# Kernel optimization log

Hardware: AMD Instinct MI355X
Metric: run time of the kernel (lower is better)

## Reference

```python
import jax, jax.numpy as jnp
import numpy as np

TOKENS, HIDDEN, N_EXPERTS = 16384, 2048, 64
JITTER_EPS = 0.01
Z_LOSS_COEFF = 0.001


def setup_inputs() -> dict:
    key = jax.random.key(0)
    k1, k2 = jax.random.split(key)
    x = jax.random.normal(k1, (TOKENS, HIDDEN), dtype=jnp.float32)
    w = jax.random.normal(k2, (N_EXPERTS, HIDDEN), dtype=jnp.float32) * 0.02  # router weight [E,H]
    return {"x": x, "w": w}


def _route_pass(scores_sel, scores, jitter_eps):
    # scores_sel: logits possibly with -inf at already-selected expert (top-2 pass)
    # scores:     original logits (used for abs/clamp factor, as in torch code)
    mx = jnp.max(scores_sel, axis=-1, keepdims=True)                      # [N,1]
    factor = jnp.maximum(jnp.abs(scores), mx)                             # scores.abs().clamp(min=mx)
    mask = jax.lax.stop_gradient((mx - scores) / factor > 2.0 * jitter_eps)
    masked_logits = jnp.where(mask, -jnp.inf, scores_sel)
    # eval path (training=False): selected_experts = argmax of (masked-for-selection) scores
    sel = jnp.argmax(scores_sel, axis=-1)[..., None]                      # [N,1] int
    gates = jax.nn.softmax(masked_logits, axis=-1)
    # mask_for_one: selected == argmax(gates) holds deterministically in eval -> 1.0
    mult = jnp.take_along_axis(gates, sel, axis=-1)                       # [N,1]
    return mult, sel


def reference(x, w):
    logits = x @ w.T                                                      # [N,E]
    # z-loss (identity on logits in forward; scalar returned for completeness)
    z_loss = Z_LOSS_COEFF * jnp.mean(jnp.square(jax.nn.logsumexp(logits, axis=-1)))
    original_gates = jax.nn.softmax(logits, axis=-1)
    # top-1 pass
    m1, s1 = _route_pass(logits, logits, JITTER_EPS)
    # top-2 pass: mask out the first selection
    e_idx = jnp.arange(logits.shape[-1])[None, :]
    scores2 = jnp.where(e_idx == s1, -jnp.inf, logits)
    m2, s2 = _route_pass(scores2, logits, JITTER_EPS)
    multiplier = jnp.concatenate([m1, m2], axis=-1)                       # [N,2]
    selected_experts = jnp.concatenate([s1, s2], axis=-1)                 # [N,2]
    return multiplier, original_gates, selected_experts, z_loss
```

## Files before the change

kernel.cpp:

```cpp
#include <hip/hip_runtime.h>
#include <math.h>

#define TOKENS 16384
#define HIDDEN 2048
#define NEXP   64
#define MT     32
#define KC     64
#define NCHUNK (HIDDEN / KC)
#define NBLK   (TOKENS / MT)

#define GATES_OFF (TOKENS * 2)
#define SEL_OFF   (GATES_OFF + TOKENS * NEXP)
#define Z_OFF     (SEL_OFF + TOKENS * 2)

#define WIMG_BYTES (NEXP * HIDDEN * 2 * 2)

typedef __attribute__((ext_vector_type(8))) _Float16 f16x8;
typedef __attribute__((ext_vector_type(4))) float    f32x4;

__device__ __forceinline__ float wave_sum64(float v) {
    #pragma unroll
    for (int s = 1; s < 64; s <<= 1) v += __shfl_xor(v, s, 64);
    return v;
}

__device__ __forceinline__ void load_lds16(const void* g, void* l) {
    __builtin_amdgcn_global_load_lds(
        (const __attribute__((address_space(1))) unsigned int*)g,
        (__attribute__((address_space(3))) unsigned int*)l, 16, 0, 0);
}

__global__ __launch_bounds__(256) void wconvert(
    const float* __restrict__ w, uint4* __restrict__ wimg)
{
    const int s = blockIdx.x * 256 + threadIdx.x;
    const int c    = s >> 10;
    const int r    = s & 1023;
    const int l    = r & 63;
    const int nt   = (r >> 6) & 1;
    const int kh   = (r >> 7) & 1;
    const int term = (r >> 8) & 1;
    const int eh   = (r >> 9) & 1;
    const int e = eh * 32 + nt * 16 + (l & 15);
    const int k = c * KC + kh * 32 + (l >> 4) * 8;

    const float* src = w + (size_t)e * HIDDEN + k;
    union { _Float16 f[8]; uint4 u; } o;
    #pragma unroll
    for (int j = 0; j < 8; ++j) {
        const float v = src[j];
        const _Float16 h = (_Float16)v;
        o.f[j] = (term == 0) ? h : (_Float16)((v - (float)h) * 4096.f);
    }
    wimg[s] = o.u;
}

__global__ __launch_bounds__(256, 3) void router_main(
    const float* __restrict__ x, const uint4* __restrict__ wimg,
    float* __restrict__ out, float* __restrict__ zpartial)
{
    __shared__ __align__(16) unsigned char lds[24576];
    __shared__ float zred[4];
    unsigned char* ldsA = lds;
    unsigned char* ldsB = lds + 8192;
    float* lg = (float*)lds;

    const int tid  = threadIdx.x;
    const int wv   = __builtin_amdgcn_readfirstlane(tid >> 6);
    const int lane = tid & 63;
    const int eh   = wv & 1;
    const int kh   = wv >> 1;
    const int t0   = blockIdx.x * MT;

    int xt[2], xq[2], aoff[2];
    #pragma unroll
    for (int p = 0; p < 2; ++p) {
        const int f = tid + 256 * p;
        const int qlo = f & 3, t = (f >> 2) & 31, qhi = f >> 7;
        const int q = qlo + 4 * qhi;
        xt[p] = t; xq[p] = q;
        const int m = t & 15, mt = t >> 4;
        const int ks2 = q >> 3;
        const int lgp = (q >> 1) & 3;
        const int j0  = 4 * (q & 1);
        const int l2  = lgp * 16 + m;
        aoff[p] = (ks2 * 2 + mt) * 1024 + l2 * 16 + j0 * 2;
    }
    const float* xrow0 = x + (size_t)(t0 + xt[0]) * HIDDEN + 4 * xq[0];
    const float* xrow1 = x + (size_t)(t0 + xt[1]) * HIDDEN + 4 * xq[1];

    const uint4* wsrc = wimg + wv * 64 + lane;
    unsigned char* wdst = ldsB + wv * 1024;

    const int aro = kh * 2048 + lane * 16;
    const int bro = eh * 8192 + kh * 2048 + lane * 16;

    f32x4 acc0[2][2], acc1[2][2];
    #pragma unroll
    for (int mt = 0; mt < 2; ++mt)
        #pragma unroll
        for (int nt = 0; nt < 2; ++nt) { acc0[mt][nt] = (f32x4)0.f; acc1[mt][nt] = (f32x4)0.f; }

    float4 curx0 = *(const float4*)(xrow0);
    float4 curx1 = *(const float4*)(xrow1);

    for (int c = 0; c < NCHUNK; ++c) {
        __syncthreads();
        #pragma unroll
        for (int p = 0; p < 4; ++p)
            load_lds16(wsrc + c * 1024 + p * 256, wdst + p * 4096);

        #pragma unroll
        for (int p = 0; p < 2; ++p) {
            const float4 v = p ? curx1 : curx0;
            union { _Float16 f[4]; uint2 u; } hh, ll;
            #pragma unroll
            for (int j = 0; j < 4; ++j) {
                const float s = (&v.x)[j];
                const _Float16 h = (_Float16)s;
                hh.f[j] = h;
                ll.f[j] = (_Float16)((s - (float)h) * 4096.f);
            }
            *(uint2*)(ldsA + aoff[p])        = hh.u;
            *(uint2*)(ldsA + aoff[p] + 4096) = ll.u;
        }
        __syncthreads();

        float4 nx0 = curx0, nx1 = curx1;
        if (c + 1 < NCHUNK) {
            nx0 = *(const float4*)(xrow0 + (c + 1) * KC);
            nx1 = *(const float4*)(xrow1 + (c + 1) * KC);
        }

        f16x8 Ah[2], Al[2], Bh[2], Bl[2];
        #pragma unroll
        for (int mt = 0; mt < 2; ++mt) {
            Ah[mt] = *(const f16x8*)(ldsA + aro + mt * 1024);
            Al[mt] = *(const f16x8*)(ldsA + aro + mt * 1024 + 4096);
        }
        #pragma unroll
        for (int nt = 0; nt < 2; ++nt) {
            Bh[nt] = *(const f16x8*)(ldsB + bro + nt * 1024);
            Bl[nt] = *(const f16x8*)(ldsB + bro + nt * 1024 + 4096);
        }
        #pragma unroll
        for (int mt = 0; mt < 2; ++mt)
            #pragma unroll
            for (int nt = 0; nt < 2; ++nt) {
                acc0[mt][nt] = __builtin_amdgcn_mfma_f32_16x16x32_f16(Ah[mt], Bh[nt], acc0[mt][nt], 0, 0, 0);
                acc1[mt][nt] = __builtin_amdgcn_mfma_f32_16x16x32_f16(Ah[mt], Bl[nt], acc1[mt][nt], 0, 0, 0);
                acc1[mt][nt] = __builtin_amdgcn_mfma_f32_16x16x32_f16(Al[mt], Bh[nt], acc1[mt][nt], 0, 0, 0);
            }

        curx0 = nx0; curx1 = nx1;
    }

    __syncthreads();
    #pragma unroll
    for (int mt = 0; mt < 2; ++mt)
        #pragma unroll
        for (int nt = 0; nt < 2; ++nt)
            #pragma unroll
            for (int r = 0; r < 4; ++r) {
                const int tok = mt * 16 + (lane >> 4) * 4 + r;
                const int e   = eh * 32 + nt * 16 + (lane & 15);
                lg[(kh * 32 + tok) * 66 + e] = acc0[mt][nt][r] + acc1[mt][nt][r] * (1.f / 4096.f);
            }
    __syncthreads();

    float zsum = 0.f;
    for (int tt = 0; tt < 8; ++tt) {
        const int t = wv * 8 + tt;
        const float v = lg[t * 66 + lane] + lg[(32 + t) * 66 + lane];

        float bv = v; int bi = lane;
        #pragma unroll
        for (int s = 1; s < 64; s <<= 1) {
            const float ov = __shfl_xor(bv, s, 64);
            const int   oi = __shfl_xor(bi, s, 64);
            if (ov > bv || (ov == bv && oi < bi)) { bv = ov; bi = oi; }
        }
        const float max1 = bv; const int s1 = bi;

        const float e1 = expf(v - max1);
        const float sume = wave_sum64(e1);
        out[GATES_OFF + (size_t)(t0 + t) * NEXP + lane] = e1 / sume;
        const float lse = max1 + logf(sume);
        zsum += lse * lse;

        const bool mask1 = (max1 - v) > 0.02f * fmaxf(fabsf(v), max1);
        const float sum1 = wave_sum64(mask1 ? 0.f : e1);

        float bv2 = (lane == s1) ? -INFINITY : v; int bi2 = lane;
        #pragma unroll
        for (int s = 1; s < 64; s <<= 1) {
            const float ov = __shfl_xor(bv2, s, 64);
            const int   oi = __shfl_xor(bi2, s, 64);
            if (ov > bv2 || (ov == bv2 && oi < bi2)) { bv2 = ov; bi2 = oi; }
        }
        const float max2 = bv2; const int s2 = bi2;

        const bool mask2 = (max2 - v) > 0.02f * fmaxf(fabsf(v), max2);
        const float p2v = (mask2 || lane == s1) ? 0.f : expf(v - max2);
        const float sum2 = wave_sum64(p2v);

        if (lane == 0) {
            const size_t trow = (size_t)(t0 + t) * 2;
            out[trow + 0] = 1.f / sum1;
            out[trow + 1] = 1.f / sum2;
            out[SEL_OFF + trow + 0] = (float)s1;
            out[SEL_OFF + trow + 1] = (float)s2;
        }
    }

    if (lane == 0) zred[wv] = zsum;
    __syncthreads();
    if (tid == 0)
        zpartial[blockIdx.x] = zred[0] + zred[1] + zred[2] + zred[3];
}

__global__ __launch_bounds__(256) void zfinal(
    const float* __restrict__ zpartial, float* __restrict__ out)
{
    const int tid = threadIdx.x;
    float v = zpartial[tid] + zpartial[tid + 256];
    v = wave_sum64(v);
    __shared__ float red[4];
    if ((tid & 63) == 0) red[tid >> 6] = v;
    __syncthreads();
    if (tid == 0) {
        const float tot = red[0] + red[1] + red[2] + red[3];
        out[Z_OFF] = 0.001f * (tot / (float)TOKENS);
    }
}

extern "C" void kernel_launch(void* const* d_in, const int* in_sizes, int n_in,
                              void* d_out, int out_size, void* d_ws, size_t ws_size,
                              hipStream_t stream) {
    const float* x = (const float*)d_in[0];
    const float* w = (const float*)d_in[1];
    float* out = (float*)d_out;

    uint4* wimg     = (uint4*)d_ws;
    float* zpartial = (float*)((char*)d_ws + WIMG_BYTES);

    wconvert<<<128, 256, 0, stream>>>(w, wimg);
    router_main<<<NBLK, 256, 0, stream>>>(x, wimg, out, zpartial);
    zfinal<<<1, 256, 0, stream>>>(zpartial, out);
}
```

Measured before the change: 228.6 us.

## Load router weights directly into registers and double-buffer the x tile in LDS

Weight fragments are no longer staged through LDS with global_load_lds. Each wave now reads its B operands straight from the pre-converted weight image into registers and prefetches the next chunk. The converted x tile is double-buffered in LDS, and x loads are prefetched two chunks ahead, which removes one of the two barriers per K-chunk and overlaps conversion with MFMA. This cuts LDS size and synchronisation, at the cost of more register pressure and uncoalesced-but-cached weight reads from L2 by every block.

```diff
diff --git a/kernel.cpp b/kernel.cpp
--- a/kernel.cpp
+++ b/kernel.cpp
@@ -22,12 +22,6 @@
     #pragma unroll
     for (int s = 1; s < 64; s <<= 1) v += __shfl_xor(v, s, 64);
     return v;
-}
-
-__device__ __forceinline__ void load_lds16(const void* g, void* l) {
-    __builtin_amdgcn_global_load_lds(
-        (const __attribute__((address_space(1))) unsigned int*)g,
-        (__attribute__((address_space(3))) unsigned int*)l, 16, 0, 0);
 }
 
 __global__ __launch_bounds__(256) void wconvert(
@@ -59,10 +53,9 @@
     const float* __restrict__ x, const uint4* __restrict__ wimg,
     float* __restrict__ out, float* __restrict__ zpartial)
 {
-    __shared__ __align__(16) unsigned char lds[24576];
+    __shared__ __align__(16) unsigned char lds[16896];
     __shared__ float zred[4];
     unsigned char* ldsA = lds;
-    unsigned char* ldsB = lds + 8192;
     float* lg = (float*)lds;
 
     const int tid  = threadIdx.x;
@@ -89,11 +82,9 @@
     const float* xrow0 = x + (size_t)(t0 + xt[0]) * HIDDEN + 4 * xq[0];
     const float* xrow1 = x + (size_t)(t0 + xt[1]) * HIDDEN + 4 * xq[1];
 
-    const uint4* wsrc = wimg + wv * 64 + lane;
-    unsigned char* wdst = ldsB + wv * 1024;
+    const uint4* wB = wimg + eh * 512 + kh * 128 + lane;
 
     const int aro = kh * 2048 + lane * 16;
-    const int bro = eh * 8192 + kh * 2048 + lane * 16;
 
     f32x4 acc0[2][2], acc1[2][2];
     #pragma unroll
@@ -101,18 +92,12 @@
         #pragma unroll
         for (int nt = 0; nt < 2; ++nt) { acc0[mt][nt] = (f32x4)0.f; acc1[mt][nt] = (f32x4)0.f; }
 
-    float4 curx0 = *(const float4*)(xrow0);
-    float4 curx1 = *(const float4*)(xrow1);
-
-    for (int c = 0; c < NCHUNK; ++c) {
-        __syncthreads();
-        #pragma unroll
-        for (int p = 0; p < 4; ++p)
-            load_lds16(wsrc + c * 1024 + p * 256, wdst + p * 4096);
-
+    {
+        const float4 v0 = *(const float4*)(xrow0);
+        const float4 v1 = *(const float4*)(xrow1);
         #pragma unroll
         for (int p = 0; p < 2; ++p) {
-            const float4 v = p ? curx1 : curx0;
+            const float4 v = p ? v1 : v0;
             union { _Float16 f[4]; uint2 u; } hh, ll;
             #pragma unroll
             for (int j = 0; j < 4; ++j) {
@@ -124,35 +109,74 @@
             *(uint2*)(ldsA + aoff[p])        = hh.u;
             *(uint2*)(ldsA + aoff[p] + 4096) = ll.u;
         }
+    }
+    float4 xA0 = *(const float4*)(xrow0 + KC);
+    float4 xA1 = *(const float4*)(xrow1 + KC);
+    f16x8 curB[2][2];
+    #pragma unroll
+    for (int t = 0; t < 2; ++t)
+        #pragma unroll
+        for (int n = 0; n < 2; ++n)
+            curB[t][n] = *reinterpret_cast<const f16x8*>(wB + t * 256 + n * 64);
+
+    for (int c = 0; c < NCHUNK; ++c) {
         __syncthreads();
-
-        float4 nx0 = curx0, nx1 = curx1;
+        const int cbuf = (c & 1) * 8192;
+        const int nbuf = 8192 - cbuf;
+
+        float4 xB0 = xA0, xB1 = xA1;
+        if (c + 2 < NCHUNK) {
+            xB0 = *(const float4*)(xrow0 + (c + 2) * KC);
+            xB1 = *(const float4*)(xrow1 + (c + 2) * KC);
+        }
+        f16x8 nxtB[2][2];
+        #pragma unroll
+        for (int t = 0; t < 2; ++t)
+            #pragma unroll
+            for (int n = 0; n < 2; ++n)
+                nxtB[t][n] = (c + 1 < NCHUNK)
+                    ? *reinterpret_cast<const f16x8*>(wB + (c + 1) * 1024 + t * 256 + n * 64)
+                    : curB[t][n];
+
+        f16x8 Ah[2], Al[2];
+        #pragma unroll
+        for (int mt = 0; mt < 2; ++mt) {
+            Ah[mt] = *(const f16x8*)(ldsA + cbuf + aro + mt * 1024);
+            Al[mt] = *(const f16x8*)(ldsA + cbuf + aro + mt * 1024 + 4096);
+        }
+
         if (c + 1 < NCHUNK) {
-            nx0 = *(const float4*)(xrow0 + (c + 1) * KC);
-            nx1 = *(const float4*)(xrow1 + (c + 1) * KC);
-        }
-
-        f16x8 Ah[2], Al[2], Bh[2], Bl[2];
-        #pragma unroll
-        for (int mt = 0; mt < 2; ++mt) {
-            Ah[mt] = *(const f16x8*)(ldsA + aro + mt * 1024);
-            Al[mt] = *(const f16x8*)(ldsA + aro + mt * 1024 + 4096);
-        }
-        #pragma unroll
-        for (int nt = 0; nt < 2; ++nt) {
-            Bh[nt] = *(const f16x8*)(ldsB + bro + nt * 1024);
-            Bl[nt] = *(const f16x8*)(ldsB + bro + nt * 1024 + 4096);
-        }
+            #pragma unroll
+            for (int p = 0; p < 2; ++p) {
+                const float4 v = p ? xA1 : xA0;
+                union { _Float16 f[4]; uint2 u; } hh, ll;
+                #pragma unroll
+                for (int j = 0; j < 4; ++j) {
+                    const float s = (&v.x)[j];
+                    const _Float16 h = (_Float16)s;
+                    hh.f[j] = h;
+                    ll.f[j] = (_Float16)((s - (float)h) * 4096.f);
+                }
+                *(uint2*)(ldsA + nbuf + aoff[p])        = hh.u;
+                *(uint2*)(ldsA + nbuf + aoff[p] + 4096) = ll.u;
+            }
+        }
+
         #pragma unroll
         for (int mt = 0; mt < 2; ++mt)
             #pragma unroll
             for (int nt = 0; nt < 2; ++nt) {
-                acc0[mt][nt] = __builtin_amdgcn_mfma_f32_16x16x32_f16(Ah[mt], Bh[nt], acc0[mt][nt], 0, 0, 0);
-                acc1[mt][nt] = __builtin_amdgcn_mfma_f32_16x16x32_f16(Ah[mt], Bl[nt], acc1[mt][nt], 0, 0, 0);
-                acc1[mt][nt] = __builtin_amdgcn_mfma_f32_16x16x32_f16(Al[mt], Bh[nt], acc1[mt][nt], 0, 0, 0);
-            }
-
-        curx0 = nx0; curx1 = nx1;
+                acc0[mt][nt] = __builtin_amdgcn_mfma_f32_16x16x32_f16(Ah[mt], curB[0][nt], acc0[mt][nt], 0, 0, 0);
+                acc1[mt][nt] = __builtin_amdgcn_mfma_f32_16x16x32_f16(Ah[mt], curB[1][nt], acc1[mt][nt], 0, 0, 0);
+                acc1[mt][nt] = __builtin_amdgcn_mfma_f32_16x16x32_f16(Al[mt], curB[0][nt], acc1[mt][nt], 0, 0, 0);
+            }
+
+        xA0 = xB0; xA1 = xB1;
+        #pragma unroll
+        for (int t = 0; t < 2; ++t)
+            #pragma unroll
+            for (int n = 0; n < 2; ++n)
+                curB[t][n] = nxtB[t][n];
     }
 
     __syncthreads();
```

Result: faster. 219.8 us (-3.9%).
